# Kernel tuning notes

Measured on AMD Instinct MI355X. Metric: run time of the kernel, lower is better.

## Reference

```python
import jax, jax.numpy as jnp
import numpy as np

N, E, IN_DIM, HID, TOWERS, NG = 20000, 320000, 16, 50, 5, 64
FO = HID // TOWERS  # out channels per tower = 10
EPS_BN = 1e-5
EPS_STD = 1e-5  # PyG StdAggregation: sqrt(relu(var) + 1e-5)


def setup_inputs() -> dict:
    key = jax.random.key(0)
    ks = jax.random.split(key, 24)
    rn = lambda k, shape: jax.random.normal(k, shape, dtype=jnp.float32) * 0.1
    F0, F1 = IN_DIM, HID
    return {
        "x": jax.random.normal(ks[0], (N, IN_DIM), dtype=jnp.float32),
        "edge_index": jax.random.randint(ks[1], (2, E), 0, N),
        "batch": jnp.sort(jax.random.randint(ks[2], (N,), 0, NG)),
        # conv0: pre Linear(2*F0 -> F0) per tower, post Linear(13*F0 -> FO) per tower, lin Linear(HID->HID)
        "pre_W0": rn(ks[3], (TOWERS, F0, 2 * F0)), "pre_b0": rn(ks[4], (TOWERS, F0)),
        "post_W0": rn(ks[5], (TOWERS, FO, 13 * F0)), "post_b0": rn(ks[6], (TOWERS, FO)),
        "lin_W0": rn(ks[7], (HID, HID)), "lin_b0": rn(ks[8], (HID,)),
        "gamma0": jnp.ones((HID,), jnp.float32), "beta0": jnp.zeros((HID,), jnp.float32),
        # conv1
        "pre_W1": rn(ks[9], (TOWERS, F1, 2 * F1)), "pre_b1": rn(ks[10], (TOWERS, F1)),
        "post_W1": rn(ks[11], (TOWERS, FO, 13 * F1)), "post_b1": rn(ks[12], (TOWERS, FO)),
        "lin_W1": rn(ks[13], (HID, HID)), "lin_b1": rn(ks[14], (HID,)),
        "gamma1": jnp.ones((HID,), jnp.float32), "beta1": jnp.zeros((HID,), jnp.float32),
        # head MLP: HID->50->25->1
        "mlp_W1": rn(ks[15], (50, HID)), "mlp_b1": rn(ks[16], (50,)),
        "mlp_W2": rn(ks[17], (25, 50)), "mlp_b2": rn(ks[18], (25,)),
        "mlp_W3": rn(ks[19], (1, 25)), "mlp_b3": rn(ks[20], (1,)),
    }


def pna_conv(x, src, dst, deg, avg_log, pre_W, pre_b, post_W, post_b, lin_W, lin_b):
    # x: [N, F]; divide_input=False -> every tower sees the full F features.
    n, Fi = x.shape
    T = pre_W.shape[0]
    # message: h = cat([x_i, x_j]) = cat([x[dst], x[src]]), then per-tower pre-MLP (1 Linear)
    h = jnp.concatenate([x[dst], x[src]], axis=-1)                  # [E, 2F]
    hs = jnp.einsum('ef,tgf->etg', h, pre_W) + pre_b                # [E, T, F]
    flat = hs.reshape(hs.shape[0], T * Fi)                          # [E, T*F]
    # multi-aggregation: mean / min / max / std, scattered to dst
    s = jax.ops.segment_sum(flat, dst, num_segments=n)
    s2 = jax.ops.segment_sum(flat * flat, dst, num_segments=n)
    mn = jax.ops.segment_min(flat, dst, num_segments=n)
    mx = jax.ops.segment_max(flat, dst, num_segments=n)
    degc = jnp.maximum(deg, 1.0)[:, None]
    mean = s / degc
    var = s2 / degc - mean * mean
    std = jnp.sqrt(jax.nn.relu(var) + EPS_STD)
    has = (deg > 0)[:, None]
    mn = jnp.where(has, mn, 0.0)
    mx = jnp.where(has, mx, 0.0)
    agg = jnp.concatenate([mean.reshape(n, T, Fi), mn.reshape(n, T, Fi),
                           mx.reshape(n, T, Fi), std.reshape(n, T, Fi)], axis=-1)  # [N,T,4F]
    # degree scalers: identity, amplification, attenuation
    amp = (jnp.log(jnp.maximum(deg, 1.0) + 1.0) / avg_log)[:, None, None]
    out = jnp.concatenate([jnp.broadcast_to(x[:, None, :], (n, T, Fi)),
                           agg, agg * amp, agg / amp], axis=-1)      # [N, T, 13F]
    out = jnp.einsum('ntf,tgf->ntg', out, post_W) + post_b          # [N, T, FO]
    return out.reshape(n, T * post_W.shape[1]) @ lin_W.T + lin_b    # [N, HID]


def _bn_relu(h, g, b):
    mu = h.mean(axis=0)
    v = jnp.mean((h - mu) ** 2, axis=0)  # biased var, torch BN training-mode normalization
    return jax.nn.relu(g * (h - mu) / jnp.sqrt(v + EPS_BN) + b)


def reference(x, edge_index, batch,
              pre_W0, pre_b0, post_W0, post_b0, lin_W0, lin_b0, gamma0, beta0,
              pre_W1, pre_b1, post_W1, post_b1, lin_W1, lin_b1, gamma1, beta1,
              mlp_W1, mlp_b1, mlp_W2, mlp_b2, mlp_W3, mlp_b3):
    src, dst = edge_index[0], edge_index[1]
    n = x.shape[0]
    deg = jax.ops.segment_sum(jnp.ones((src.shape[0],), jnp.float32), dst, num_segments=n)
    avg_log = jnp.mean(jnp.log(deg + 1.0))  # PNA avg_deg['log'] from this graph's degree histogram
    # NOTE: zip(convs, batch_norms) in the torch forward applies only num_conv_layer=2 convs.
    h = pna_conv(x, src, dst, deg, avg_log, pre_W0, pre_b0, post_W0, post_b0, lin_W0, lin_b0)
    h = _bn_relu(h, gamma0, beta0)
    h = pna_conv(h, src, dst, deg, avg_log, pre_W1, pre_b1, post_W1, post_b1, lin_W1, lin_b1)
    h = _bn_relu(h, gamma1, beta1)
    cnt = jax.ops.segment_sum(jnp.ones((n,), jnp.float32), batch, num_segments=NG)
    pooled = jax.ops.segment_sum(h, batch, num_segments=NG) / jnp.maximum(cnt, 1.0)[:, None]
    h = jax.nn.relu(pooled @ mlp_W1.T + mlp_b1)
    h = jax.nn.relu(h @ mlp_W2.T + mlp_b2)
    return h @ mlp_W3.T + mlp_b3  # [NG, 1]
```

## Files before the change

### kernel.cpp

```cpp
#include <hip/hip_runtime.h>
#include <math.h>
#include <float.h>

#define NN 20000
#define EE 320000
#define INDIM 16
#define HID 50
#define TW 5
#define FO 10
#define NGROUPS 64

typedef float f4 __attribute__((ext_vector_type(4)));
typedef float f2 __attribute__((ext_vector_type(2)));

__device__ inline f4 f4_min(f4 a, f4 b) {
    f4 r; r.x = fminf(a.x, b.x); r.y = fminf(a.y, b.y);
    r.z = fminf(a.z, b.z); r.w = fminf(a.w, b.w); return r;
}
__device__ inline f4 f4_max(f4 a, f4 b) {
    f4 r; r.x = fmaxf(a.x, b.x); r.y = fmaxf(a.y, b.y);
    r.z = fmaxf(a.z, b.z); r.w = fmaxf(a.w, b.w); return r;
}
__device__ inline float sh3sum(float v, int g0, int G_) {
    return v + __shfl(v, g0 + G_, 64) + __shfl(v, g0 + 2 * G_, 64);
}
__device__ inline float sh3min(float v, int g0, int G_) {
    return fminf(fminf(v, __shfl(v, g0 + G_, 64)), __shfl(v, g0 + 2 * G_, 64));
}
__device__ inline float sh3max(float v, int g0, int G_) {
    return fmaxf(fmaxf(v, __shfl(v, g0 + G_, 64)), __shfl(v, g0 + 2 * G_, 64));
}
__device__ inline void acc4(float& acc, f4 w, float a0, float a1, float a2, float a3) {
    acc += w.x * a0; acc += w.y * a1; acc += w.z * a2; acc += w.w * a3;
}

__global__ void k_deg(const int* __restrict__ dst, int* __restrict__ deg) {
    int e = blockIdx.x * 256 + threadIdx.x;
    if (e < EE) atomicAdd(&deg[dst[e]], 1);
}

__global__ void k_scan(const int* __restrict__ deg, int* __restrict__ offsets,
                       float* __restrict__ scal) {
    __shared__ int part[1024];
    __shared__ float fred[1024];
    const int CH = 20;
    int tid = threadIdx.x;
    int base = tid * CH;
    int loc[CH];
    int s = 0; float fs = 0.f;
    for (int c = 0; c < CH; ++c) {
        int idx = base + c;
        int v = (idx < NN) ? deg[idx] : 0;
        loc[c] = s; s += v;
        if (idx < NN) fs += logf((float)v + 1.0f);
    }
    part[tid] = s; fred[tid] = fs; __syncthreads();
    for (int off = 1; off < 1024; off <<= 1) {
        int v = (tid >= off) ? part[tid - off] : 0;
        __syncthreads();
        part[tid] += v;
        __syncthreads();
    }
    int pre = (tid > 0) ? part[tid - 1] : 0;
    for (int c = 0; c < CH; ++c) {
        int idx = base + c;
        if (idx < NN) offsets[idx] = pre + loc[c];
    }
    if (tid == 0) offsets[NN] = part[1023];
    for (int off = 512; off > 0; off >>= 1) {
        if (tid < off) fred[tid] += fred[tid + off];
        __syncthreads();
    }
    if (tid == 0) scal[0] = fred[0] / (float)NN;
}

__global__ void k_fill(const int* __restrict__ src, const int* __restrict__ dst,
                       const int* __restrict__ offsets, int* __restrict__ cursor,
                       int* __restrict__ csr_src) {
    int e = blockIdx.x * 256 + threadIdx.x;
    if (e < EE) {
        int d = dst[e];
        int pos = offsets[d] + atomicAdd(&cursor[d], 1);
        csr_src[pos] = src[e];
    }
}

__global__ void k_pack(const float* __restrict__ preW0, const float* __restrict__ preW1,
                       const float* __restrict__ postW0, const float* __restrict__ postW1,
                       const float* __restrict__ linW0, const float* __restrict__ linW1,
                       float* __restrict__ preWt0, float* __restrict__ preWt1,
                       float* __restrict__ Wx0, float* __restrict__ Wid0,
                       float* __restrict__ Wamp0, float* __restrict__ Watt0,
                       float* __restrict__ Wx1, float* __restrict__ Wid1,
                       float* __restrict__ Wamp1, float* __restrict__ Watt1,
                       float* __restrict__ Lt0, float* __restrict__ Lt1) {
    int idx = blockIdx.x * 256 + threadIdx.x;
    int job = blockIdx.y;
    int q = idx >> 8, k = (idx >> 2) & 63, j = idx & 3;
    switch (job) {
    case 0:
        if (idx < 32 * 80) { int c = idx / 80, r = idx % 80; preWt0[idx] = preW0[r * 32 + c]; }
        break;
    case 1:
        if (idx < 100 * 256) { int c = idx / 256, r = idx % 256; preWt1[idx] = (r < 250) ? preW1[r * 100 + c] : 0.f; }
        break;
    case 2:
        if (idx < 4 * 256) { int f = q * 4 + j; Wx0[idx] = (k < HID) ? postW0[k * 208 + f] : 0.f; }
        break;
    case 3:
        if (idx < 16 * 256) { int s = q / 4, f = (q % 4) * 4 + j; Wid0[idx] = (k < HID) ? postW0[k * 208 + (1 + s) * 16 + f] : 0.f; }
        break;
    case 4:
        if (idx < 16 * 256) { int s = q / 4, f = (q % 4) * 4 + j; Wamp0[idx] = (k < HID) ? postW0[k * 208 + (5 + s) * 16 + f] : 0.f; }
        break;
    case 5:
        if (idx < 16 * 256) { int s = q / 4, f = (q % 4) * 4 + j; Watt0[idx] = (k < HID) ? postW0[k * 208 + (9 + s) * 16 + f] : 0.f; }
        break;
    case 6:
        if (idx < 13 * 256) { int f = q * 4 + j; Wx1[idx] = (f < 50 && k < HID) ? postW1[k * 650 + f] : 0.f; }
        break;
    case 7:
        if (idx < 52 * 256) { int s = q / 13, f = (q % 13) * 4 + j; Wid1[idx] = (f < 50 && k < HID) ? postW1[k * 650 + (1 + s) * 50 + f] : 0.f; }
        break;
    case 8:
        if (idx < 52 * 256) { int s = q / 13, f = (q % 13) * 4 + j; Wamp1[idx] = (f < 50 && k < HID) ? postW1[k * 650 + (5 + s) * 50 + f] : 0.f; }
        break;
    case 9:
        if (idx < 52 * 256) { int s = q / 13, f = (q % 13) * 4 + j; Watt1[idx] = (f < 50 && k < HID) ? postW1[k * 650 + (9 + s) * 50 + f] : 0.f; }
        break;
    case 10:
        if (idx < 13 * 256) { int f = q * 4 + j; Lt0[idx] = (f < 50 && k < HID) ? linW0[k * 50 + f] : 0.f; }
        break;
    case 11:
        if (idx < 13 * 256) { int f = q * 4 + j; Lt1[idx] = (f < 50 && k < HID) ? linW1[k * 50 + f] : 0.f; }
        break;
    }
}

template <int F, int TF, int TFP>
__global__ __launch_bounds__(256, 4) void k_gemm_CP(
    const float* __restrict__ x, const float* __restrict__ preWt,
    const float* __restrict__ b,
    float* __restrict__ C, float* __restrict__ P) {
    const int NODES = 16;
    __shared__ float xs[NODES * F];
    int tid = threadIdx.x;
    int base = blockIdx.x * NODES;
    for (int idx = tid; idx < NODES * F; idx += 256) xs[idx] = x[(size_t)base * F + idx];
    __syncthreads();
    if (tid < TF) {
        float accC[NODES], accP[NODES];
#pragma unroll
        for (int n = 0; n < NODES; ++n) { accC[n] = 0.f; accP[n] = 0.f; }
        for (int f = 0; f < F; ++f) {
            float wl = preWt[f * TFP + tid];
            float wr = preWt[(F + f) * TFP + tid];
#pragma unroll
            for (int n = 0; n < NODES; ++n) {
                float xv = xs[n * F + f];
                accC[n] += xv * wl;
                accP[n] += xv * wr;
            }
        }
        float bb = b[tid];
        for (int n = 0; n < NODES; ++n) {
            C[((size_t)(base + n)) * TFP + tid] = accC[n] + bb;
            P[((size_t)(base + n)) * TFP + tid] = accP[n];
        }
    } else if (tid < TFP) {
        for (int n = 0; n < NODES; ++n) {
            C[((size_t)(base + n)) * TFP + tid] = 0.f;
            P[((size_t)(base + n)) * TFP + tid] = 0.f;
        }
    }
}

template <int F, int TFP, int EP, int XSTR>
__global__ __launch_bounds__(256) void k_gather(
    const float* __restrict__ xin, const float* __restrict__ C, const float* __restrict__ P,
    const int* __restrict__ offsets, const int* __restrict__ csr,
    float* __restrict__ agg, float* __restrict__ xp) {
    const int G = TFP / 4;
    int t = threadIdx.x;
    int w = t >> 6, lane = t & 63;
    int i = blockIdx.x * 4 + w;
    int beg = offsets[i], end = offsets[i + 1];
    int d = end - beg;
    int g = (EP == 1) ? lane : (lane % G);
    int e = (EP == 1) ? 0 : (lane / G);
    bool act = (EP == 1) ? (g < G) : (e < EP);
    f4 S = {0.f, 0.f, 0.f, 0.f}, S2 = {0.f, 0.f, 0.f, 0.f};
    f4 MN = {FLT_MAX, FLT_MAX, FLT_MAX, FLT_MAX};
    f4 MX = {-FLT_MAX, -FLT_MAX, -FLT_MAX, -FLT_MAX};
    const f4* __restrict__ Pv = (const f4*)P;
    if (act) {
        if (EP == 1) {
            int j = beg;
            for (; j + 4 <= end; j += 4) {
                int s0 = csr[j], s1 = csr[j + 1], s2 = csr[j + 2], s3 = csr[j + 3];
                f4 a = Pv[(size_t)s0 * G + g];
                f4 b = Pv[(size_t)s1 * G + g];
                f4 c = Pv[(size_t)s2 * G + g];
                f4 dd = Pv[(size_t)s3 * G + g];
                S += a; S2 += a * a; MN = f4_min(MN, a); MX = f4_max(MX, a);
                S += b; S2 += b * b; MN = f4_min(MN, b); MX = f4_max(MX, b);
                S += c; S2 += c * c; MN = f4_min(MN, c); MX = f4_max(MX, c);
                S += dd; S2 += dd * dd; MN = f4_min(MN, dd); MX = f4_max(MX, dd);
            }
            for (; j < end; ++j) {
                int s0 = csr[j];
                f4 a = Pv[(size_t)s0 * G + g];
                S += a; S2 += a * a; MN = f4_min(MN, a); MX = f4_max(MX, a);
            }
        } else {
            int j = beg + e;
            for (; j + EP < end; j += 2 * EP) {
                int s0 = csr[j], s1 = csr[j + EP];
                f4 a = Pv[(size_t)s0 * G + g];
                f4 b = Pv[(size_t)s1 * G + g];
                S += a; S2 += a * a; MN = f4_min(MN, a); MX = f4_max(MX, a);
                S += b; S2 += b * b; MN = f4_min(MN, b); MX = f4_max(MX, b);
            }
            if (j < end) {
                int s0 = csr[j];
                f4 a = Pv[(size_t)s0 * G + g];
                S += a; S2 += a * a; MN = f4_min(MN, a); MX = f4_max(MX, a);
            }
        }
    }
    if (EP == 3) {
        int g0 = lane % G;
        S.x = sh3sum(S.x, g0, G); S.y = sh3sum(S.y, g0, G);
        S.z = sh3sum(S.z, g0, G); S.w = sh3sum(S.w, g0, G);
        S2.x = sh3sum(S2.x, g0, G); S2.y = sh3sum(S2.y, g0, G);
        S2.z = sh3sum(S2.z, g0, G); S2.w = sh3sum(S2.w, g0, G);
        MN.x = sh3min(MN.x, g0, G); MN.y = sh3min(MN.y, g0, G);
        MN.z = sh3min(MN.z, g0, G); MN.w = sh3min(MN.w, g0, G);
        MX.x = sh3max(MX.x, g0, G); MX.y = sh3max(MX.y, g0, G);
        MX.z = sh3max(MX.z, g0, G); MX.w = sh3max(MX.w, g0, G);
    }
    if (lane < G) {
        f4 Cv = ((const f4*)C)[(size_t)i * G + lane];
        float degf = (float)d;
        float rdegc = 1.0f / fmaxf(degf, 1.0f);
        f4 mean, sq, var, stdv, mnv, mxv;
        mean.x = (degf * Cv.x + S.x) * rdegc; mean.y = (degf * Cv.y + S.y) * rdegc;
        mean.z = (degf * Cv.z + S.z) * rdegc; mean.w = (degf * Cv.w + S.w) * rdegc;
        sq.x = degf * Cv.x * Cv.x + 2.f * Cv.x * S.x + S2.x;
        sq.y = degf * Cv.y * Cv.y + 2.f * Cv.y * S.y + S2.y;
        sq.z = degf * Cv.z * Cv.z + 2.f * Cv.z * S.z + S2.z;
        sq.w = degf * Cv.w * Cv.w + 2.f * Cv.w * S.w + S2.w;
        var.x = sq.x * rdegc - mean.x * mean.x; var.y = sq.y * rdegc - mean.y * mean.y;
        var.z = sq.z * rdegc - mean.z * mean.z; var.w = sq.w * rdegc - mean.w * mean.w;
        stdv.x = sqrtf(fmaxf(var.x, 0.f) + 1e-5f); stdv.y = sqrtf(fmaxf(var.y, 0.f) + 1e-5f);
        stdv.z = sqrtf(fmaxf(var.z, 0.f) + 1e-5f); stdv.w = sqrtf(fmaxf(var.w, 0.f) + 1e-5f);
        if (d > 0) {
            mnv.x = Cv.x + MN.x; mnv.y = Cv.y + MN.y; mnv.z = Cv.z + MN.z; mnv.w = Cv.w + MN.w;
            mxv.x = Cv.x + MX.x; mxv.y = Cv.y + MX.y; mxv.z = Cv.z + MX.z; mxv.w = Cv.w + MX.w;
        } else {
            mnv = (f4){0.f, 0.f, 0.f, 0.f}; mxv = mnv;
        }
        f4* __restrict__ dstv = (f4*)(agg + (size_t)i * 4 * TFP);
        dstv[lane] = mean;
        dstv[G + lane] = mnv;
        dstv[2 * G + lane] = mxv;
        dstv[3 * G + lane] = stdv;
    }
    if (XSTR > 0 && lane < XSTR)
        xp[(size_t)i * XSTR + lane] = (lane < F) ? xin[(size_t)i * F + lane] : 0.f;
}

template <int F, int TFP, int SQ, int SQX, int XSTR, bool AF4>
__global__ __launch_bounds__(128) void k_post(
    const float* __restrict__ xsrc, const float* __restrict__ agg,
    const int* __restrict__ offsets, const float* __restrict__ scal,
    const float* __restrict__ Wx, const float* __restrict__ Wid,
    const float* __restrict__ Wamp, const float* __restrict__ Watt,
    const float* __restrict__ postb,
    const float* __restrict__ Lt, const float* __restrict__ linb,
    float* __restrict__ hout) {
    __shared__ __align__(16) float sY[2][8][52];
    int t = threadIdx.x;
    int w = t >> 6, lane = t & 63;
    int base = blockIdx.x * 16 + w * 8;
    int kk = (lane < HID) ? lane : (HID - 1);
    int tw = kk / FO;
    float rscal = 1.0f / scal[0];
    float amp[8], ia[8];
#pragma unroll
    for (int n = 0; n < 8; ++n) {
        int dd = offsets[base + n + 1] - offsets[base + n];
        float a = logf(fmaxf((float)dd, 1.f) + 1.f) * rscal;
        amp[n] = a; ia[n] = 1.0f / a;
    }
    float y0[8], y1[8], y2[8];
#pragma unroll
    for (int n = 0; n < 8; ++n) { y0[n] = 0.f; y1[n] = 0.f; y2[n] = 0.f; }
    const f4* __restrict__ Wxv = (const f4*)Wx;
    const f4* __restrict__ Wiv = (const f4*)Wid;
    const f4* __restrict__ Wav = (const f4*)Wamp;
    const f4* __restrict__ Wtv = (const f4*)Watt;
    for (int q = 0; q < SQX; ++q) {
        f4 wv = Wxv[q * 64 + lane];
#pragma unroll
        for (int n = 0; n < 8; ++n) {
            f4 a = *(const f4*)(xsrc + (size_t)(base + n) * XSTR + 4 * q);
            acc4(y0[n], wv, a.x, a.y, a.z, a.w);
        }
    }
    for (int s = 0; s < 4; ++s) {
        for (int q = 0; q < SQ; ++q) {
            f4 wi = Wiv[(s * SQ + q) * 64 + lane];
            f4 wa = Wav[(s * SQ + q) * 64 + lane];
            f4 wt = Wtv[(s * SQ + q) * 64 + lane];
#pragma unroll
            for (int n = 0; n < 8; ++n) {
                const float* __restrict__ Ab =
                    agg + ((size_t)(base + n) * 4 + s) * TFP + tw * F + 4 * q;
                float a0, a1, a2, a3;
                if constexpr (AF4) {
                    f4 av = *(const f4*)Ab;
                    a0 = av.x; a1 = av.y; a2 = av.z; a3 = av.w;
                } else {
                    f2 u = *(const f2*)Ab;
                    f2 v = *(const f2*)(Ab + 2);
                    a0 = u.x; a1 = u.y; a2 = v.x; a3 = v.y;
                }
                acc4(y0[n], wi, a0, a1, a2, a3);
                acc4(y1[n], wa, a0, a1, a2, a3);
                acc4(y2[n], wt, a0, a1, a2, a3);
            }
        }
    }
    float pb = postb[kk];
#pragma unroll
    for (int n = 0; n < 8; ++n) {
        float y = pb + y0[n] + amp[n] * y1[n] + ia[n] * y2[n];
        if (lane < HID) sY[w][n][lane] = y;
        else if (lane < 52) sY[w][n][lane] = 0.f;
    }
    const f4* __restrict__ Lv = (const f4*)Lt;
    float o[8];
    float lb = linb[kk];
#pragma unroll
    for (int n = 0; n < 8; ++n) o[n] = lb;
    for (int q = 0; q < 13; ++q) {
        f4 lv = Lv[q * 64 + lane];
#pragma unroll
        for (int n = 0; n < 8; ++n) {
            f4 sv = *(const f4*)(&sY[w][n][4 * q]);
            acc4(o[n], lv, sv.x, sv.y, sv.z, sv.w);
        }
    }
    if (lane < HID) {
#pragma unroll
        for (int n = 0; n < 8; ++n)
            hout[(size_t)(base + n) * HID + lane] = o[n];
    }
}

__global__ void k_bn_part(const float* __restrict__ h, float* __restrict__ acc) {
    __shared__ float ss[4][64], ss2[4][64];
    int t = threadIdx.x;
    int rs = t >> 6, c = t & 63;
    float s = 0.f, s2 = 0.f;
    if (c < HID) {
        int r0 = blockIdx.x * 200 + rs;
        int rend = blockIdx.x * 200 + 200;
        if (rend > NN) rend = NN;
        for (int r = r0; r < rend; r += 4) {
            float v = h[(size_t)r * HID + c];
            s += v; s2 += v * v;
        }
    }
    ss[rs][c] = s; ss2[rs][c] = s2;
    __syncthreads();
    if (t < HID) {
        float S = ss[0][t] + ss[1][t] + ss[2][t] + ss[3][t];
        float S2 = ss2[0][t] + ss2[1][t] + ss2[2][t] + ss2[3][t];
        atomicAdd(&acc[t], S);
        atomicAdd(&acc[64 + t], S2);
    }
}

__global__ void k_bn_relu(const float* __restrict__ hin, const float* __restrict__ acc,
                          const float* __restrict__ gamma, const float* __restrict__ beta,
                          float* __restrict__ hout) {
    int idx = blockIdx.x * 256 + threadIdx.x;
    if (idx < NN * HID) {
        int c = idx % HID;
        float mu = acc[c] * (1.f / NN);
        float var = acc[64 + c] * (1.f / NN) - mu * mu;
        float v = hin[idx];
        hout[idx] = fmaxf(gamma[c] * (v - mu) * rsqrtf(var + 1e-5f) + beta[c], 0.f);
    }
}

__global__ void k_head(const float* __restrict__ h, const int* __restrict__ batch,
                       const float* __restrict__ W1, const float* __restrict__ b1,
                       const float* __restrict__ W2, const float* __restrict__ b2,
                       const float* __restrict__ W3, const float* __restrict__ b3,
                       float* __restrict__ out) {
    __shared__ float sp[HID], h1[50], h2[25];
    __shared__ int sbound[2];
    int g = blockIdx.x, tid = threadIdx.x;
    if (tid < 2) {
        int target = g + tid;
        int lo = 0, hi = NN;
        while (lo < hi) {
            int mid = (lo + hi) >> 1;
            if (batch[mid] < target) lo = mid + 1; else hi = mid;
        }
        sbound[tid] = lo;
    }
    __syncthreads();
    int beg = sbound[0], end = sbound[1];
    if (tid < HID) {
        float s0 = 0.f, s1 = 0.f, s2 = 0.f, s3 = 0.f;
        int n = beg;
        for (; n + 4 <= end; n += 4) {
            s0 += h[(size_t)n * HID + tid];
            s1 += h[(size_t)(n + 1) * HID + tid];
            s2 += h[(size_t)(n + 2) * HID + tid];
            s3 += h[(size_t)(n + 3) * HID + tid];
        }
        for (; n < end; ++n) s0 += h[(size_t)n * HID + tid];
        sp[tid] = (s0 + s1 + s2 + s3) / fmaxf((float)(end - beg), 1.0f);
    }
    __syncthreads();
    if (tid < 50) {
        float a = b1[tid];
        for (int k = 0; k < HID; ++k) a += W1[tid * HID + k] * sp[k];
        h1[tid] = fmaxf(a, 0.f);
    }
    __syncthreads();
    if (tid < 25) {
        float a = b2[tid];
        for (int k = 0; k < 50; ++k) a += W2[tid * 50 + k] * h1[k];
        h2[tid] = fmaxf(a, 0.f);
    }
    __syncthreads();
    if (tid == 0) {
        float a = b3[0];
        for (int k = 0; k < 25; ++k) a += W3[k] * h2[k];
        out[g] = a;
    }
}

extern "C" void kernel_launch(void* const* d_in, const int* in_sizes, int n_in,
                              void* d_out, int out_size, void* d_ws, size_t ws_size,
                              hipStream_t stream) {
    const float* x      = (const float*)d_in[0];
    const int*   ei     = (const int*)d_in[1];
    const int*   batch  = (const int*)d_in[2];
    const float* preW0  = (const float*)d_in[3];
    const float* preb0  = (const float*)d_in[4];
    const float* postW0 = (const float*)d_in[5];
    const float* postb0 = (const float*)d_in[6];
    const float* linW0  = (const float*)d_in[7];
    const float* linb0  = (const float*)d_in[8];
    const float* gamma0 = (const float*)d_in[9];
    const float* beta0  = (const float*)d_in[10];
    const float* preW1  = (const float*)d_in[11];
    const float* preb1  = (const float*)d_in[12];
    const float* postW1 = (const float*)d_in[13];
    const float* postb1 = (const float*)d_in[14];
    const float* linW1  = (const float*)d_in[15];
    const float* linb1  = (const float*)d_in[16];
    const float* gamma1 = (const float*)d_in[17];
    const float* beta1  = (const float*)d_in[18];
    const float* mW1    = (const float*)d_in[19];
    const float* mb1    = (const float*)d_in[20];
    const float* mW2    = (const float*)d_in[21];
    const float* mb2    = (const float*)d_in[22];
    const float* mW3    = (const float*)d_in[23];
    const float* mb3    = (const float*)d_in[24];
    float* out = (float*)d_out;
    (void)in_sizes; (void)n_in; (void)out_size; (void)ws_size;

    char* ws = (char*)d_ws;
    size_t off = 0;
    auto alloc = [&](size_t bytes) -> void* {
        void* p = ws + off;
        off += (bytes + 255) & ~(size_t)255;
        return p;
    };
    int*   deg     = (int*)alloc((size_t)NN * 4);
    int*   offsets = (int*)alloc((size_t)(NN + 1) * 4);
    int*   cursor  = (int*)alloc((size_t)NN * 4);
    int*   csr_src = (int*)alloc((size_t)EE * 4);
    float* scal    = (float*)alloc(64);
    float* bnacc0  = (float*)alloc(128 * 4);
    float* bnacc1  = (float*)alloc(128 * 4);
    float* preWt0  = (float*)alloc((size_t)32 * 80 * 4);
    float* preWt1  = (float*)alloc((size_t)100 * 256 * 4);
    float* Wx0     = (float*)alloc((size_t)4 * 256 * 4);
    float* Wid0    = (float*)alloc((size_t)16 * 256 * 4);
    float* Wamp0   = (float*)alloc((size_t)16 * 256 * 4);
    float* Watt0   = (float*)alloc((size_t)16 * 256 * 4);
    float* Wx1     = (float*)alloc((size_t)13 * 256 * 4);
    float* Wid1    = (float*)alloc((size_t)52 * 256 * 4);
    float* Wamp1   = (float*)alloc((size_t)52 * 256 * 4);
    float* Watt1   = (float*)alloc((size_t)52 * 256 * 4);
    float* Lt0     = (float*)alloc((size_t)13 * 256 * 4);
    float* Lt1     = (float*)alloc((size_t)13 * 256 * 4);
    float* Cbuf    = (float*)alloc((size_t)NN * 256 * 4);
    float* Pbuf    = (float*)alloc((size_t)NN * 256 * 4);
    float* h1buf   = (float*)alloc((size_t)NN * HID * 4);
    float* h2buf   = (float*)alloc((size_t)NN * HID * 4);
    float* aggbuf  = (float*)alloc((size_t)NN * 4 * 256 * 4);
    float* xp      = (float*)alloc((size_t)NN * 52 * 4);

    const int* src = ei;
    const int* dst = ei + EE;

    hipMemsetAsync(deg, 0, (size_t)NN * 4, stream);
    hipMemsetAsync(cursor, 0, (size_t)NN * 4, stream);
    hipMemsetAsync(bnacc0, 0, 128 * 4, stream);
    hipMemsetAsync(bnacc1, 0, 128 * 4, stream);

    k_pack<<<dim3(100, 12), 256, 0, stream>>>(preW0, preW1, postW0, postW1, linW0, linW1,
                                              preWt0, preWt1, Wx0, Wid0, Wamp0, Watt0,
                                              Wx1, Wid1, Wamp1, Watt1, Lt0, Lt1);
    k_deg<<<EE / 256, 256, 0, stream>>>(dst, deg);
    k_scan<<<1, 1024, 0, stream>>>(deg, offsets, scal);
    k_fill<<<EE / 256, 256, 0, stream>>>(src, dst, offsets, cursor, csr_src);

    k_gemm_CP<INDIM, 80, 80><<<NN / 16, 256, 0, stream>>>(x, preWt0, preb0, Cbuf, Pbuf);
    k_gather<INDIM, 80, 3, 0><<<NN / 4, 256, 0, stream>>>(x, Cbuf, Pbuf, offsets, csr_src,
                                                          aggbuf, xp);
    k_post<INDIM, 80, 4, 4, 16, true><<<NN / 16, 128, 0, stream>>>(
        x, aggbuf, offsets, scal, Wx0, Wid0, Wamp0, Watt0, postb0, Lt0, linb0, h1buf);
    k_bn_part<<<100, 256, 0, stream>>>(h1buf, bnacc0);
    k_bn_relu<<<(NN * HID + 255) / 256, 256, 0, stream>>>(h1buf, bnacc0, gamma0, beta0, h1buf);

    k_gemm_CP<HID, 250, 256><<<NN / 16, 256, 0, stream>>>(h1buf, preWt1, preb1, Cbuf, Pbuf);
    k_gather<HID, 256, 1, 52><<<NN / 4, 256, 0, stream>>>(h1buf, Cbuf, Pbuf, offsets, csr_src,
                                                          aggbuf, xp);
    k_post<HID, 256, 13, 13, 52, false><<<NN / 16, 128, 0, stream>>>(
        xp, aggbuf, offsets, scal, Wx1, Wid1, Wamp1, Watt1, postb1, Lt1, linb1, h2buf);
    k_bn_part<<<100, 256, 0, stream>>>(h2buf, bnacc1);
    k_bn_relu<<<(NN * HID + 255) / 256, 256, 0, stream>>>(h2buf, bnacc1, gamma1, beta1, h2buf);

    k_head<<<NGROUPS, 64, 0, stream>>>(h2buf, batch, mW1, mb1, mW2, mb2, mW3, mb3, out);
}
```

Baseline: 384.6 us.

## Fuse gather, post-MLP and BN stats into one conv kernel; defer BN-ReLU to consumers

```diff
diff --git a/kernel.cpp b/kernel.cpp
--- a/kernel.cpp
+++ b/kernel.cpp
@@ -137,16 +137,27 @@
     }
 }
 
-template <int F, int TF, int TFP>
+template <int F, int TF, int TFP, bool BN>
 __global__ __launch_bounds__(256, 4) void k_gemm_CP(
     const float* __restrict__ x, const float* __restrict__ preWt,
     const float* __restrict__ b,
+    const float* __restrict__ bnacc, const float* __restrict__ gam,
+    const float* __restrict__ bet,
     float* __restrict__ C, float* __restrict__ P) {
     const int NODES = 16;
     __shared__ float xs[NODES * F];
     int tid = threadIdx.x;
     int base = blockIdx.x * NODES;
-    for (int idx = tid; idx < NODES * F; idx += 256) xs[idx] = x[(size_t)base * F + idx];
+    for (int idx = tid; idx < NODES * F; idx += 256) {
+        float v = x[(size_t)base * F + idx];
+        if (BN) {
+            int c = idx % F;
+            float mu = bnacc[c] * (1.f / NN);
+            float var = bnacc[64 + c] * (1.f / NN) - mu * mu;
+            v = fmaxf(gam[c] * (v - mu) * rsqrtf(var + 1e-5f) + bet[c], 0.f);
+        }
+        xs[idx] = v;
+    }
     __syncthreads();
     if (tid < TF) {
         float accC[NODES], accP[NODES];
@@ -175,228 +186,193 @@
     }
 }
 
-template <int F, int TFP, int EP, int XSTR>
-__global__ __launch_bounds__(256) void k_gather(
+template <int F, int TFPG, int TFPL, int EP, int SQ, int SQX, bool AF4, bool BNIN>
+__global__ __launch_bounds__(512, 6) void k_conv(
     const float* __restrict__ xin, const float* __restrict__ C, const float* __restrict__ P,
     const int* __restrict__ offsets, const int* __restrict__ csr,
-    float* __restrict__ agg, float* __restrict__ xp) {
-    const int G = TFP / 4;
-    int t = threadIdx.x;
-    int w = t >> 6, lane = t & 63;
-    int i = blockIdx.x * 4 + w;
+    const float* __restrict__ scal,
+    const float* __restrict__ Wx, const float* __restrict__ Wid,
+    const float* __restrict__ Wamp, const float* __restrict__ Watt,
+    const float* __restrict__ postb, const float* __restrict__ Lt,
+    const float* __restrict__ linb,
+    const float* __restrict__ bn_in, const float* __restrict__ g_in,
+    const float* __restrict__ b_in,
+    float* __restrict__ hout, float* __restrict__ bn_out) {
+    const int GP = TFPG / 4;
+    const int GL = TFPL / 4;
+    __shared__ __align__(16) float sAgg[8][5][TFPL];
+    __shared__ __align__(16) float sY[8][52];
+    int t = threadIdx.x, w = t >> 6, lane = t & 63;
+    int i = blockIdx.x * 8 + w;
     int beg = offsets[i], end = offsets[i + 1];
     int d = end - beg;
-    int g = (EP == 1) ? lane : (lane % G);
-    int e = (EP == 1) ? 0 : (lane / G);
-    bool act = (EP == 1) ? (g < G) : (e < EP);
-    f4 S = {0.f, 0.f, 0.f, 0.f}, S2 = {0.f, 0.f, 0.f, 0.f};
-    f4 MN = {FLT_MAX, FLT_MAX, FLT_MAX, FLT_MAX};
-    f4 MX = {-FLT_MAX, -FLT_MAX, -FLT_MAX, -FLT_MAX};
-    const f4* __restrict__ Pv = (const f4*)P;
-    if (act) {
-        if (EP == 1) {
-            int j = beg;
-            for (; j + 4 <= end; j += 4) {
-                int s0 = csr[j], s1 = csr[j + 1], s2 = csr[j + 2], s3 = csr[j + 3];
-                f4 a = Pv[(size_t)s0 * G + g];
-                f4 b = Pv[(size_t)s1 * G + g];
-                f4 c = Pv[(size_t)s2 * G + g];
-                f4 dd = Pv[(size_t)s3 * G + g];
-                S += a; S2 += a * a; MN = f4_min(MN, a); MX = f4_max(MX, a);
-                S += b; S2 += b * b; MN = f4_min(MN, b); MX = f4_max(MX, b);
-                S += c; S2 += c * c; MN = f4_min(MN, c); MX = f4_max(MX, c);
-                S += dd; S2 += dd * dd; MN = f4_min(MN, dd); MX = f4_max(MX, dd);
+
+    {
+        int g = (EP == 1) ? lane : (lane % GL);
+        int e = (EP == 1) ? 0 : (lane / GL);
+        bool act = (EP == 1) ? (lane < GL) : (e < EP);
+        f4 S = {0.f, 0.f, 0.f, 0.f}, S2 = {0.f, 0.f, 0.f, 0.f};
+        f4 MN = {FLT_MAX, FLT_MAX, FLT_MAX, FLT_MAX};
+        f4 MX = {-FLT_MAX, -FLT_MAX, -FLT_MAX, -FLT_MAX};
+        const f4* __restrict__ Pv = (const f4*)P;
+        if (act) {
+            if (EP == 1) {
+                int j = beg;
+                for (; j + 4 <= end; j += 4) {
+                    int s0 = csr[j], s1 = csr[j + 1], s2 = csr[j + 2], s3 = csr[j + 3];
+                    f4 a = Pv[(size_t)s0 * GP + g];
+                    f4 b = Pv[(size_t)s1 * GP + g];
+                    f4 c = Pv[(size_t)s2 * GP + g];
+                    f4 dd = Pv[(size_t)s3 * GP + g];
+                    S += a; S2 += a * a; MN = f4_min(MN, a); MX = f4_max(MX, a);
+                    S += b; S2 += b * b; MN = f4_min(MN, b); MX = f4_max(MX, b);
+                    S += c; S2 += c * c; MN = f4_min(MN, c); MX = f4_max(MX, c);
+                    S += dd; S2 += dd * dd; MN = f4_min(MN, dd); MX = f4_max(MX, dd);
+                }
+                for (; j < end; ++j) {
+                    int s0 = csr[j];
+                    f4 a = Pv[(size_t)s0 * GP + g];
+                    S += a; S2 += a * a; MN = f4_min(MN, a); MX = f4_max(MX, a);
+                }
+            } else {
+                int j = beg + e;
+                for (; j + EP < end; j += 2 * EP) {
+                    int s0 = csr[j], s1 = csr[j + EP];
+                    f4 a = Pv[(size_t)s0 * GP + g];
+                    f4 b = Pv[(size_t)s1 * GP + g];
+                    S += a; S2 += a * a; MN = f4_min(MN, a); MX = f4_max(MX, a);
+                    S += b; S2 += b * b; MN = f4_min(MN, b); MX = f4_max(MX, b);
+                }
+                if (j < end) {
+                    int s0 = csr[j];
+                    f4 a = Pv[(size_t)s0 * GP + g];
+                    S += a; S2 += a * a; MN = f4_min(MN, a); MX = f4_max(MX, a);
+                }
             }
-            for (; j < end; ++j) {
-                int s0 = csr[j];
-                f4 a = Pv[(size_t)s0 * G + g];
-                S += a; S2 += a * a; MN = f4_min(MN, a); MX = f4_max(MX, a);
+        }
+        if (EP == 3) {
+            int g0 = lane % GL;
+            S.x = sh3sum(S.x, g0, GL); S.y = sh3sum(S.y, g0, GL);
+            S.z = sh3sum(S.z, g0, GL); S.w = sh3sum(S.w, g0, GL);
+            S2.x = sh3sum(S2.x, g0, GL); S2.y = sh3sum(S2.y, g0, GL);
+            S2.z = sh3sum(S2.z, g0, GL); S2.w = sh3sum(S2.w, g0, GL);
+            MN.x = sh3min(MN.x, g0, GL); MN.y = sh3min(MN.y, g0, GL);
+            MN.z = sh3min(MN.z, g0, GL); MN.w = sh3min(MN.w, g0, GL);
+            MX.x = sh3max(MX.x, g0, GL); MX.y = sh3max(MX.y, g0, GL);
+            MX.z = sh3max(MX.z, g0, GL); MX.w = sh3max(MX.w, g0, GL);
+        }
+        if (lane < GL) {
+            f4 Cv = ((const f4*)C)[(size_t)i * GP + lane];
+            float degf = (float)d;
+            float rdegc = 1.0f / fmaxf(degf, 1.0f);
+            f4 mean, sq, var, stdv, mnv, mxv;
+            mean.x = (degf * Cv.x + S.x) * rdegc; mean.y = (degf * Cv.y + S.y) * rdegc;
+            mean.z = (degf * Cv.z + S.z) * rdegc; mean.w = (degf * Cv.w + S.w) * rdegc;
+            sq.x = degf * Cv.x * Cv.x + 2.f * Cv.x * S.x + S2.x;
+            sq.y = degf * Cv.y * Cv.y + 2.f * Cv.y * S.y + S2.y;
+            sq.z = degf * Cv.z * Cv.z + 2.f * Cv.z * S.z + S2.z;
+            sq.w = degf * Cv.w * Cv.w + 2.f * Cv.w * S.w + S2.w;
+            var.x = sq.x * rdegc - mean.x * mean.x; var.y = sq.y * rdegc - mean.y * mean.y;
+            var.z = sq.z * rdegc - mean.z * mean.z; var.w = sq.w * rdegc - mean.w * mean.w;
+            stdv.x = sqrtf(fmaxf(var.x, 0.f) + 1e-5f); stdv.y = sqrtf(fmaxf(var.y, 0.f) + 1e-5f);
+            stdv.z = sqrtf(fmaxf(var.z, 0.f) + 1e-5f); stdv.w = sqrtf(fmaxf(var.w, 0.f) + 1e-5f);
+            if (d > 0) {
+                mnv.x = Cv.x + MN.x; mnv.y = Cv.y + MN.y; mnv.z = Cv.z + MN.z; mnv.w = Cv.w + MN.w;
+                mxv.x = Cv.x + MX.x; mxv.y = Cv.y + MX.y; mxv.z = Cv.z + MX.z; mxv.w = Cv.w + MX.w;
+            } else {
+                mnv = (f4){0.f, 0.f, 0.f, 0.f}; mxv = mnv;
             }
-        } else {
-            int j = beg + e;
-            for (; j + EP < end; j += 2 * EP) {
-                int s0 = csr[j], s1 = csr[j + EP];
-                f4 a = Pv[(size_t)s0 * G + g];
-                f4 b = Pv[(size_t)s1 * G + g];
-                S += a; S2 += a * a; MN = f4_min(MN, a); MX = f4_max(MX, a);
-                S += b; S2 += b * b; MN = f4_min(MN, b); MX = f4_max(MX, b);
-            }
-            if (j < end) {
-                int s0 = csr[j];
-                f4 a = Pv[(size_t)s0 * G + g];
-                S += a; S2 += a * a; MN = f4_min(MN, a); MX = f4_max(MX, a);
-            }
-        }
-    }
-    if (EP == 3) {
-        int g0 = lane % G;
-        S.x = sh3sum(S.x, g0, G); S.y = sh3sum(S.y, g0, G);
-        S.z = sh3sum(S.z, g0, G); S.w = sh3sum(S.w, g0, G);
-        S2.x = sh3sum(S2.x, g0, G); S2.y = sh3sum(S2.y, g0, G);
-        S2.z = sh3sum(S2.z, g0, G); S2.w = sh3sum(S2.w, g0, G);
-        MN.x = sh3min(MN.x, g0, G); MN.y = sh3min(MN.y, g0, G);
-        MN.z = sh3min(MN.z, g0, G); MN.w = sh3min(MN.w, g0, G);
-        MX.x = sh3max(MX.x, g0, G); MX.y = sh3max(MX.y, g0, G);
-        MX.z = sh3max(MX.z, g0, G); MX.w = sh3max(MX.w, g0, G);
-    }
-    if (lane < G) {
-        f4 Cv = ((const f4*)C)[(size_t)i * G + lane];
-        float degf = (float)d;
-        float rdegc = 1.0f / fmaxf(degf, 1.0f);
-        f4 mean, sq, var, stdv, mnv, mxv;
-        mean.x = (degf * Cv.x + S.x) * rdegc; mean.y = (degf * Cv.y + S.y) * rdegc;
-        mean.z = (degf * Cv.z + S.z) * rdegc; mean.w = (degf * Cv.w + S.w) * rdegc;
-        sq.x = degf * Cv.x * Cv.x + 2.f * Cv.x * S.x + S2.x;
-        sq.y = degf * Cv.y * Cv.y + 2.f * Cv.y * S.y + S2.y;
-        sq.z = degf * Cv.z * Cv.z + 2.f * Cv.z * S.z + S2.z;
-        sq.w = degf * Cv.w * Cv.w + 2.f * Cv.w * S.w + S2.w;
-        var.x = sq.x * rdegc - mean.x * mean.x; var.y = sq.y * rdegc - mean.y * mean.y;
-        var.z = sq.z * rdegc - mean.z * mean.z; var.w = sq.w * rdegc - mean.w * mean.w;
-        stdv.x = sqrtf(fmaxf(var.x, 0.f) + 1e-5f); stdv.y = sqrtf(fmaxf(var.y, 0.f) + 1e-5f);
-        stdv.z = sqrtf(fmaxf(var.z, 0.f) + 1e-5f); stdv.w = sqrtf(fmaxf(var.w, 0.f) + 1e-5f);
-        if (d > 0) {
-            mnv.x = Cv.x + MN.x; mnv.y = Cv.y + MN.y; mnv.z = Cv.z + MN.z; mnv.w = Cv.w + MN.w;
-            mxv.x = Cv.x + MX.x; mxv.y = Cv.y + MX.y; mxv.z = Cv.z + MX.z; mxv.w = Cv.w + MX.w;
-        } else {
-            mnv = (f4){0.f, 0.f, 0.f, 0.f}; mxv = mnv;
-        }
-        f4* __restrict__ dstv = (f4*)(agg + (size_t)i * 4 * TFP);
-        dstv[lane] = mean;
-        dstv[G + lane] = mnv;
-        dstv[2 * G + lane] = mxv;
-        dstv[3 * G + lane] = stdv;
-    }
-    if (XSTR > 0 && lane < XSTR)
-        xp[(size_t)i * XSTR + lane] = (lane < F) ? xin[(size_t)i * F + lane] : 0.f;
-}
-
-template <int F, int TFP, int SQ, int SQX, int XSTR, bool AF4>
-__global__ __launch_bounds__(128) void k_post(
-    const float* __restrict__ xsrc, const float* __restrict__ agg,
-    const int* __restrict__ offsets, const float* __restrict__ scal,
-    const float* __restrict__ Wx, const float* __restrict__ Wid,
-    const float* __restrict__ Wamp, const float* __restrict__ Watt,
-    const float* __restrict__ postb,
-    const float* __restrict__ Lt, const float* __restrict__ linb,
-    float* __restrict__ hout) {
-    __shared__ __align__(16) float sY[2][8][52];
-    int t = threadIdx.x;
-    int w = t >> 6, lane = t & 63;
-    int base = blockIdx.x * 16 + w * 8;
+            ((f4*)&sAgg[w][0][0])[lane] = mean;
+            ((f4*)&sAgg[w][1][0])[lane] = mnv;
+            ((f4*)&sAgg[w][2][0])[lane] = mxv;
+            ((f4*)&sAgg[w][3][0])[lane] = stdv;
+        }
+    }
+    if (BNIN) {
+        if (lane < F) {
+            float hv = xin[(size_t)i * F + lane];
+            float mu = bn_in[lane] * (1.f / NN);
+            float var = bn_in[64 + lane] * (1.f / NN) - mu * mu;
+            sAgg[w][4][lane] = fmaxf(g_in[lane] * (hv - mu) * rsqrtf(var + 1e-5f) + b_in[lane], 0.f);
+        } else if (lane < SQX * 4) {
+            sAgg[w][4][lane] = 0.f;
+        }
+    } else {
+        if (lane < F) sAgg[w][4][lane] = xin[(size_t)i * F + lane];
+        else if (lane < SQX * 4) sAgg[w][4][lane] = 0.f;
+    }
+    float amp = logf(fmaxf((float)d, 1.f) + 1.f) / scal[0];
+    float ia = 1.0f / amp;
+    __syncthreads();
+
     int kk = (lane < HID) ? lane : (HID - 1);
     int tw = kk / FO;
-    float rscal = 1.0f / scal[0];
-    float amp[8], ia[8];
-#pragma unroll
-    for (int n = 0; n < 8; ++n) {
-        int dd = offsets[base + n + 1] - offsets[base + n];
-        float a = logf(fmaxf((float)dd, 1.f) + 1.f) * rscal;
-        amp[n] = a; ia[n] = 1.0f / a;
-    }
-    float y0[8], y1[8], y2[8];
-#pragma unroll
-    for (int n = 0; n < 8; ++n) { y0[n] = 0.f; y1[n] = 0.f; y2[n] = 0.f; }
     const f4* __restrict__ Wxv = (const f4*)Wx;
     const f4* __restrict__ Wiv = (const f4*)Wid;
     const f4* __restrict__ Wav = (const f4*)Wamp;
     const f4* __restrict__ Wtv = (const f4*)Watt;
+    float y0 = 0.f, y1 = 0.f, y2 = 0.f;
+#pragma unroll
     for (int q = 0; q < SQX; ++q) {
         f4 wv = Wxv[q * 64 + lane];
+        f4 a = *(const f4*)(&sAgg[w][4][4 * q]);
+        acc4(y0, wv, a.x, a.y, a.z, a.w);
+    }
 #pragma unroll
-        for (int n = 0; n < 8; ++n) {
-            f4 a = *(const f4*)(xsrc + (size_t)(base + n) * XSTR + 4 * q);
-            acc4(y0[n], wv, a.x, a.y, a.z, a.w);
-        }
-    }
     for (int s = 0; s < 4; ++s) {
+        const float* __restrict__ A = &sAgg[w][s][tw * F];
+#pragma unroll 4
         for (int q = 0; q < SQ; ++q) {
             f4 wi = Wiv[(s * SQ + q) * 64 + lane];
             f4 wa = Wav[(s * SQ + q) * 64 + lane];
             f4 wt = Wtv[(s * SQ + q) * 64 + lane];
+            float a0, a1, a2, a3;
+            if constexpr (AF4) {
+                f4 av = *(const f4*)(A + 4 * q);
+                a0 = av.x; a1 = av.y; a2 = av.z; a3 = av.w;
+            } else {
+                f2 u = *(const f2*)(A + 4 * q);
+                f2 v = *(const f2*)(A + 4 * q + 2);
+                a0 = u.x; a1 = u.y; a2 = v.x; a3 = v.y;
+            }
+            acc4(y0, wi, a0, a1, a2, a3);
+            acc4(y1, wa, a0, a1, a2, a3);
+            acc4(y2, wt, a0, a1, a2, a3);
+        }
+    }
+    float y = postb[kk] + y0 + amp * y1 + ia * y2;
+    if (lane < HID) sY[w][lane] = y;
+    else if (lane < 52) sY[w][lane] = 0.f;
+
+    const f4* __restrict__ Lv = (const f4*)Lt;
+    float o = linb[kk];
 #pragma unroll
-            for (int n = 0; n < 8; ++n) {
-                const float* __restrict__ Ab =
-                    agg + ((size_t)(base + n) * 4 + s) * TFP + tw * F + 4 * q;
-                float a0, a1, a2, a3;
-                if constexpr (AF4) {
-                    f4 av = *(const f4*)Ab;
-                    a0 = av.x; a1 = av.y; a2 = av.z; a3 = av.w;
-                } else {
-                    f2 u = *(const f2*)Ab;
-                    f2 v = *(const f2*)(Ab + 2);
-                    a0 = u.x; a1 = u.y; a2 = v.x; a3 = v.y;
-                }
-                acc4(y0[n], wi, a0, a1, a2, a3);
-                acc4(y1[n], wa, a0, a1, a2, a3);
-                acc4(y2[n], wt, a0, a1, a2, a3);
-            }
-        }
-    }
-    float pb = postb[kk];
-#pragma unroll
-    for (int n = 0; n < 8; ++n) {
-        float y = pb + y0[n] + amp[n] * y1[n] + ia[n] * y2[n];
-        if (lane < HID) sY[w][n][lane] = y;
-        else if (lane < 52) sY[w][n][lane] = 0.f;
-    }
-    const f4* __restrict__ Lv = (const f4*)Lt;
-    float o[8];
-    float lb = linb[kk];
-#pragma unroll
-    for (int n = 0; n < 8; ++n) o[n] = lb;
     for (int q = 0; q < 13; ++q) {
         f4 lv = Lv[q * 64 + lane];
+        f4 sv = *(const f4*)(&sY[w][4 * q]);
+        acc4(o, lv, sv.x, sv.y, sv.z, sv.w);
+    }
+    if (lane < HID) hout[(size_t)i * HID + lane] = o;
+
+    float ov = (lane < HID) ? o : 0.f;
+    sAgg[w][0][lane] = ov;
+    sAgg[w][1][lane] = ov * ov;
+    __syncthreads();
+    if (t < 64 && lane < HID) {
+        float s = 0.f, s2 = 0.f;
 #pragma unroll
-        for (int n = 0; n < 8; ++n) {
-            f4 sv = *(const f4*)(&sY[w][n][4 * q]);
-            acc4(o[n], lv, sv.x, sv.y, sv.z, sv.w);
-        }
-    }
-    if (lane < HID) {
-#pragma unroll
-        for (int n = 0; n < 8; ++n)
-            hout[(size_t)(base + n) * HID + lane] = o[n];
-    }
-}
-
-__global__ void k_bn_part(const float* __restrict__ h, float* __restrict__ acc) {
-    __shared__ float ss[4][64], ss2[4][64];
-    int t = threadIdx.x;
-    int rs = t >> 6, c = t & 63;
-    float s = 0.f, s2 = 0.f;
-    if (c < HID) {
-        int r0 = blockIdx.x * 200 + rs;
-        int rend = blockIdx.x * 200 + 200;
-        if (rend > NN) rend = NN;
-        for (int r = r0; r < rend; r += 4) {
-            float v = h[(size_t)r * HID + c];
-            s += v; s2 += v * v;
-        }
-    }
-    ss[rs][c] = s; ss2[rs][c] = s2;
-    __syncthreads();
-    if (t < HID) {
-        float S = ss[0][t] + ss[1][t] + ss[2][t] + ss[3][t];
-        float S2 = ss2[0][t] + ss2[1][t] + ss2[2][t] + ss2[3][t];
-        atomicAdd(&acc[t], S);
-        atomicAdd(&acc[64 + t], S2);
-    }
-}
-
-__global__ void k_bn_relu(const float* __restrict__ hin, const float* __restrict__ acc,
-                          const float* __restrict__ gamma, const float* __restrict__ beta,
-                          float* __restrict__ hout) {
-    int idx = blockIdx.x * 256 + threadIdx.x;
-    if (idx < NN * HID) {
-        int c = idx % HID;
-        float mu = acc[c] * (1.f / NN);
-        float var = acc[64 + c] * (1.f / NN) - mu * mu;
-        float v = hin[idx];
-        hout[idx] = fmaxf(gamma[c] * (v - mu) * rsqrtf(var + 1e-5f) + beta[c], 0.f);
+        for (int w2 = 0; w2 < 8; ++w2) {
+            s += sAgg[w2][0][lane];
+            s2 += sAgg[w2][1][lane];
+        }
+        atomicAdd(&bn_out[lane], s);
+        atomicAdd(&bn_out[64 + lane], s2);
     }
 }
 
 __global__ void k_head(const float* __restrict__ h, const int* __restrict__ batch,
+                       const float* __restrict__ bnacc, const float* __restrict__ gam,
+                       const float* __restrict__ bet,
                        const float* __restrict__ W1, const float* __restrict__ b1,
                        const float* __restrict__ W2, const float* __restrict__ b2,
                        const float* __restrict__ W3, const float* __restrict__ b3,
@@ -416,15 +392,19 @@
     __syncthreads();
     int beg = sbound[0], end = sbound[1];
     if (tid < HID) {
+        float mu = bnacc[tid] * (1.f / NN);
+        float var = bnacc[64 + tid] * (1.f / NN) - mu * mu;
+        float sc = gam[tid] * rsqrtf(var + 1e-5f);
+        float sh = bet[tid] - mu * sc;
         float s0 = 0.f, s1 = 0.f, s2 = 0.f, s3 = 0.f;
         int n = beg;
         for (; n + 4 <= end; n += 4) {
-            s0 += h[(size_t)n * HID + tid];
-            s1 += h[(size_t)(n + 1) * HID + tid];
-            s2 += h[(size_t)(n + 2) * HID + tid];
-            s3 += h[(size_t)(n + 3) * HID + tid];
-        }
-        for (; n < end; ++n) s0 += h[(size_t)n * HID + tid];
+            s0 += fmaxf(fmaf(h[(size_t)n * HID + tid], sc, sh), 0.f);
+            s1 += fmaxf(fmaf(h[(size_t)(n + 1) * HID + tid], sc, sh), 0.f);
+            s2 += fmaxf(fmaf(h[(size_t)(n + 2) * HID + tid], sc, sh), 0.f);
+            s3 += fmaxf(fmaf(h[(size_t)(n + 3) * HID + tid], sc, sh), 0.f);
+        }
+        for (; n < end; ++n) s0 += fmaxf(fmaf(h[(size_t)n * HID + tid], sc, sh), 0.f);
         sp[tid] = (s0 + s1 + s2 + s3) / fmaxf((float)(end - beg), 1.0f);
     }
     __syncthreads();
@@ -486,12 +466,13 @@
         return p;
     };
     int*   deg     = (int*)alloc((size_t)NN * 4);
+    int*   cursor  = (int*)alloc((size_t)NN * 4);
+    float* bnacc0  = (float*)alloc(128 * 4);
+    float* bnacc1  = (float*)alloc(128 * 4);
+    size_t zero_bytes = off;
     int*   offsets = (int*)alloc((size_t)(NN + 1) * 4);
-    int*   cursor  = (int*)alloc((size_t)NN * 4);
     int*   csr_src = (int*)alloc((size_t)EE * 4);
     float* scal    = (float*)alloc(64);
-    float* bnacc0  = (float*)alloc(128 * 4);
-    float* bnacc1  = (float*)alloc(128 * 4);
     float* preWt0  = (float*)alloc((size_t)32 * 80 * 4);
     float* preWt1  = (float*)alloc((size_t)100 * 256 * 4);
     float* Wx0     = (float*)alloc((size_t)4 * 256 * 4);
@@ -508,16 +489,11 @@
     float* Pbuf    = (float*)alloc((size_t)NN * 256 * 4);
     float* h1buf   = (float*)alloc((size_t)NN * HID * 4);
     float* h2buf   = (float*)alloc((size_t)NN * HID * 4);
-    float* aggbuf  = (float*)alloc((size_t)NN * 4 * 256 * 4);
-    float* xp      = (float*)alloc((size_t)NN * 52 * 4);
 
     const int* src = ei;
     const int* dst = ei + EE;
 
-    hipMemsetAsync(deg, 0, (size_t)NN * 4, stream);
-    hipMemsetAsync(cursor, 0, (size_t)NN * 4, stream);
-    hipMemsetAsync(bnacc0, 0, 128 * 4, stream);
-    hipMemsetAsync(bnacc1, 0, 128 * 4, stream);
+    hipMemsetAsync(ws, 0, zero_bytes, stream);
 
     k_pack<<<dim3(100, 12), 256, 0, stream>>>(preW0, preW1, postW0, postW1, linW0, linW1,
                                               preWt0, preWt1, Wx0, Wid0, Wamp0, Watt0,
@@ -526,21 +502,18 @@
     k_scan<<<1, 1024, 0, stream>>>(deg, offsets, scal);
     k_fill<<<EE / 256, 256, 0, stream>>>(src, dst, offsets, cursor, csr_src);
 
-    k_gemm_CP<INDIM, 80, 80><<<NN / 16, 256, 0, stream>>>(x, preWt0, preb0, Cbuf, Pbuf);
-    k_gather<INDIM, 80, 3, 0><<<NN / 4, 256, 0, stream>>>(x, Cbuf, Pbuf, offsets, csr_src,
-                                                          aggbuf, xp);
-    k_post<INDIM, 80, 4, 4, 16, true><<<NN / 16, 128, 0, stream>>>(
-        x, aggbuf, offsets, scal, Wx0, Wid0, Wamp0, Watt0, postb0, Lt0, linb0, h1buf);
-    k_bn_part<<<100, 256, 0, stream>>>(h1buf, bnacc0);
-    k_bn_relu<<<(NN * HID + 255) / 256, 256, 0, stream>>>(h1buf, bnacc0, gamma0, beta0, h1buf);
-
-    k_gemm_CP<HID, 250, 256><<<NN / 16, 256, 0, stream>>>(h1buf, preWt1, preb1, Cbuf, Pbuf);
-    k_gather<HID, 256, 1, 52><<<NN / 4, 256, 0, stream>>>(h1buf, Cbuf, Pbuf, offsets, csr_src,
-                                                          aggbuf, xp);
-    k_post<HID, 256, 13, 13, 52, false><<<NN / 16, 128, 0, stream>>>(
-        xp, aggbuf, offsets, scal, Wx1, Wid1, Wamp1, Watt1, postb1, Lt1, linb1, h2buf);
-    k_bn_part<<<100, 256, 0, stream>>>(h2buf, bnacc1);
-    k_bn_relu<<<(NN * HID + 255) / 256, 256, 0, stream>>>(h2buf, bnacc1, gamma1, beta1, h2buf);
-
-    k_head<<<NGROUPS, 64, 0, stream>>>(h2buf, batch, mW1, mb1, mW2, mb2, mW3, mb3, out);
-}
+    k_gemm_CP<INDIM, 80, 80, false><<<NN / 16, 256, 0, stream>>>(
+        x, preWt0, preb0, nullptr, nullptr, nullptr, Cbuf, Pbuf);
+    k_conv<INDIM, 80, 80, 3, 4, 4, true, false><<<NN / 8, 512, 0, stream>>>(
+        x, Cbuf, Pbuf, offsets, csr_src, scal, Wx0, Wid0, Wamp0, Watt0, postb0, Lt0, linb0,
+        nullptr, nullptr, nullptr, h1buf, bnacc0);
+
+    k_gemm_CP<HID, 250, 256, true><<<NN / 16, 256, 0, stream>>>(
+        h1buf, preWt1, preb1, bnacc0, gamma0, beta0, Cbuf, Pbuf);
+    k_conv<HID, 256, 252, 1, 13, 13, false, true><<<NN / 8, 512, 0, stream>>>(
+        h1buf, Cbuf, Pbuf, offsets, csr_src, scal, Wx1, Wid1, Wamp1, Watt1, postb1, Lt1, linb1,
+        bnacc0, gamma0, beta0, h2buf, bnacc1);
+
+    k_head<<<NGROUPS, 64, 0, stream>>>(h2buf, batch, bnacc1, gamma1, beta1,
+                                       mW1, mb1, mW2, mb2, mW3, mb3, out);
+}
```

Result: faster. 344.7 us (-10.4%).
